# Optimization experiments

Hardware: AMD Instinct MI355X
Metric: run time of the kernel (lower is better)

Reference implementation:

```python
import jax, jax.numpy as jnp
import numpy as np

RES = 7          # pooler_resolution
SR = 2           # sampling_ratio
SCALES = (0.25, 0.125, 0.0625)  # 1/stride for the 3 FPN levels


def _bilinear(feat, ys, xs):
    # feat [C,H,W]; ys, xs [N,S,S] sample coords; returns [C,N,S,S]
    C, H, W = feat.shape
    valid = (ys > -1.0) & (ys < H) & (xs > -1.0) & (xs < W)
    y = jnp.clip(ys, 0.0, H - 1)
    x = jnp.clip(xs, 0.0, W - 1)
    y0 = jnp.floor(y).astype(jnp.int32)
    x0 = jnp.floor(x).astype(jnp.int32)
    y1 = jnp.minimum(y0 + 1, H - 1)
    x1 = jnp.minimum(x0 + 1, W - 1)
    ly = y - y0; lx = x - x0
    hy = 1.0 - ly; hx = 1.0 - lx
    v = (feat[:, y0, x0] * (hy * hx) + feat[:, y0, x1] * (hy * lx)
         + feat[:, y1, x0] * (ly * hx) + feat[:, y1, x1] * (ly * lx))
    return v * valid


def _roi_align(feat, boxes, scale):
    # feat [C,H,W], boxes [N,4] (t,l,b,r) in image coords, aligned=True
    t, l, b, r = (boxes[:, 0], boxes[:, 1], boxes[:, 2], boxes[:, 3])
    sy = t * scale - 0.5
    sx = l * scale - 0.5
    bh = (b - t) * scale / RES
    bw = (r - l) * scale / RES
    S = RES * SR
    g = (jnp.arange(S, dtype=feat.dtype) + 0.5) / SR  # sample offsets in bin units
    ys = sy[:, None] + g[None, :] * bh[:, None]  # [N,S]
    xs = sx[:, None] + g[None, :] * bw[:, None]
    N = boxes.shape[0]
    Y = jnp.broadcast_to(ys[:, :, None], (N, S, S))
    X = jnp.broadcast_to(xs[:, None, :], (N, S, S))
    v = _bilinear(feat, Y, X)                      # [C,N,S,S]
    C = feat.shape[0]
    v = v.reshape(C, N, RES, SR, RES, SR).mean(axis=(3, 5))
    return jnp.transpose(v, (1, 0, 2, 3))          # [N,C,RES,RES]


def _forward(feat0, feat1, feat2, bbox2d, anchor_id,
             fc1_w, fc1_b, bn1_g, bn1_b, fc2_w, fc2_b, bn2_g, bn2_b,
             cate_w, cate_b, bbox3d_w, bbox3d_b, yawc_w, yawc_b,
             yawr_w, yawr_b, hgt_w, hgt_b):
    # yxhw -> tlbr (mu.convert_box_format_yxhw_to_tlbr)
    cy, cx, h, w = (bbox2d[..., 0], bbox2d[..., 1], bbox2d[..., 2], bbox2d[..., 3])
    tlbr = jnp.stack([cy - h / 2, cx - w / 2, cy + h / 2, cx + w / 2], axis=-1)
    level = anchor_id // 3  # [B,N] per-box FPN level (anchor_id // 3 == i routing)
    feats = [feat0, feat1, feat2]
    B, N = level.shape
    C = feat0.shape[1]
    pooled = jnp.zeros((B, N, C, RES, RES), dtype=feat0.dtype)
    for i in range(3):
        al = jax.vmap(lambda fm, bx, s=SCALES[i]: _roi_align(fm, bx, s))(feats[i], tlbr)
        pooled = jnp.where((level == i)[:, :, None, None, None], al, pooled)
    x = pooled.reshape(B * N, -1)  # [B*N, C*RES*RES]
    eps = 1e-5
    for Wt, bb, g2, b2 in ((fc1_w, fc1_b, bn1_g, bn1_b), (fc2_w, fc2_b, bn2_g, bn2_b)):
        x = x @ Wt + bb
        mu = x.mean(0)
        var = x.var(0)
        x = jax.nn.relu((x - mu) / jnp.sqrt(var + eps) * g2 + b2)
    cate = x @ cate_w + cate_b
    bbox3d = x @ bbox3d_w + bbox3d_b
    yawc = x @ yawc_w + yawc_b
    yawr = x @ yawr_w + yawr_b
    hgt = x @ hgt_w + hgt_b
    out = jnp.concatenate([cate, bbox3d, yawc, yawr, hgt], axis=-1)  # [B*N, 100]
    return out.reshape(B, N, -1)


def setup_inputs() -> dict:
    key = jax.random.key(0)
    ks = jax.random.split(key, 24)
    B, N, C = 4, 512, 256
    FC = 1024
    IMG = 512.0
    NUM_CLASSES, BOX_DIM, BINS = 3, 6, 12
    feat0 = jax.random.normal(ks[0], (B, C, 128, 128), jnp.float32)
    feat1 = jax.random.normal(ks[1], (B, C, 64, 64), jnp.float32)
    feat2 = jax.random.normal(ks[2], (B, C, 32, 32), jnp.float32)
    cy = jax.random.uniform(ks[3], (B, N)) * IMG
    cx = jax.random.uniform(ks[4], (B, N)) * IMG
    h = 16.0 + jax.random.uniform(ks[5], (B, N)) * 240.0
    w = 16.0 + jax.random.uniform(ks[6], (B, N)) * 240.0
    bbox2d = jnp.stack([cy, cx, h, w], axis=-1)
    anchor_id = jax.random.randint(ks[7], (B, N), 0, 9, dtype=jnp.int32)
    in_dim = C * RES * RES  # 12544
    fc1_w = jax.random.normal(ks[8], (in_dim, FC), jnp.float32) / np.sqrt(in_dim)
    fc1_b = jnp.zeros((FC,), jnp.float32)
    bn1_g = jnp.ones((FC,), jnp.float32)
    bn1_b = jnp.zeros((FC,), jnp.float32)
    fc2_w = jax.random.normal(ks[9], (FC, FC), jnp.float32) / np.sqrt(FC)
    fc2_b = jnp.zeros((FC,), jnp.float32)
    bn2_g = jnp.ones((FC,), jnp.float32)
    bn2_b = jnp.zeros((FC,), jnp.float32)
    cate_w = jax.random.normal(ks[10], (FC, NUM_CLASSES + 1), jnp.float32) * 0.01
    cate_b = jnp.zeros((NUM_CLASSES + 1,), jnp.float32)
    bbox3d_w = jax.random.normal(ks[11], (FC, NUM_CLASSES * BOX_DIM), jnp.float32) * 0.001
    bbox3d_b = jnp.zeros((NUM_CLASSES * BOX_DIM,), jnp.float32)
    yawc_w = jax.random.normal(ks[12], (FC, NUM_CLASSES * BINS), jnp.float32) * 0.001
    yawc_b = jnp.zeros((NUM_CLASSES * BINS,), jnp.float32)
    yawr_w = jax.random.normal(ks[13], (FC, NUM_CLASSES * BINS), jnp.float32) * 0.001
    yawr_b = jnp.zeros((NUM_CLASSES * BINS,), jnp.float32)
    hgt_w = jax.random.normal(ks[14], (FC, NUM_CLASSES * 2), jnp.float32) * 0.001
    hgt_b = jnp.zeros((NUM_CLASSES * 2,), jnp.float32)
    return {
        'feat0': feat0, 'feat1': feat1, 'feat2': feat2,
        'bbox2d': bbox2d, 'anchor_id': anchor_id,
        'fc1_w': fc1_w, 'fc1_b': fc1_b, 'bn1_g': bn1_g, 'bn1_b': bn1_b,
        'fc2_w': fc2_w, 'fc2_b': fc2_b, 'bn2_g': bn2_g, 'bn2_b': bn2_b,
        'cate_w': cate_w, 'cate_b': cate_b, 'bbox3d_w': bbox3d_w, 'bbox3d_b': bbox3d_b,
        'yawc_w': yawc_w, 'yawc_b': yawc_b, 'yawr_w': yawr_w, 'yawr_b': yawr_b,
        'hgt_w': hgt_w, 'hgt_b': hgt_b,
    }


def reference(feat0, feat1, feat2, bbox2d, anchor_id,
              fc1_w, fc1_b, bn1_g, bn1_b, fc2_w, fc2_b, bn2_g, bn2_b,
              cate_w, cate_b, bbox3d_w, bbox3d_b, yawc_w, yawc_b,
              yawr_w, yawr_b, hgt_w, hgt_b):
    return _forward(feat0, feat1, feat2, bbox2d, anchor_id,
                    fc1_w, fc1_b, bn1_g, bn1_b, fc2_w, fc2_b, bn2_g, bn2_b,
                    cate_w, cate_b, bbox3d_w, bbox3d_b, yawc_w, yawc_b,
                    yawr_w, yawr_b, hgt_w, hgt_b)
```

## Files before the change

kernel.cpp:

```cpp
#include <hip/hip_runtime.h>
#include <hip/hip_bf16.h>

typedef unsigned short u16;
typedef unsigned int u32;
typedef __bf16 bf16x8 __attribute__((ext_vector_type(8)));
typedef float f32x4 __attribute__((ext_vector_type(4)));

#define RESOLUTION 7
#define SR 2
#define SS 14
#define NSAMP 196

static __device__ __forceinline__ u16 f2bf(float f) {
    __hip_bfloat16 t = __float2bfloat16(f);
    return *reinterpret_cast<u16*>(&t);
}
static __device__ __forceinline__ float bf2f(u16 h) {
    return __uint_as_float(((u32)h) << 16);
}

static __device__ __forceinline__ void load_lds16(const u16* g, u16* l) {
    __builtin_amdgcn_global_load_lds(
        (const __attribute__((address_space(1))) unsigned int*)g,
        (__attribute__((address_space(3))) unsigned int*)l, 16, 0, 0);
}

__global__ __launch_bounds__(256) void transpose_feat3_kernel(
    const float* __restrict__ f0, const float* __restrict__ f1,
    const float* __restrict__ f2, u16* __restrict__ tf0,
    u16* __restrict__ tf1, u16* __restrict__ tf2) {
    int b = blockIdx.y;
    int bx = blockIdx.x;
    const float* in;
    u16* out;
    int HW, hw0;
    if (bx < 256)      { in = f0; out = tf0; HW = 16384; hw0 = bx * 64; }
    else if (bx < 320) { in = f1; out = tf1; HW = 4096;  hw0 = (bx - 256) * 64; }
    else               { in = f2; out = tf2; HW = 1024;  hw0 = (bx - 320) * 64; }

    __shared__ u16 tile[256][65];
    int hw4 = (threadIdx.x & 15) * 4;
    int cs = threadIdx.x >> 4;
    for (int cc = 0; cc < 256; cc += 16) {
        int c = cc + cs;
        float4 v = *(const float4*)&in[((size_t)(b * 256 + c)) * HW + hw0 + hw4];
        tile[c][hw4 + 0] = f2bf(v.x);
        tile[c][hw4 + 1] = f2bf(v.y);
        tile[c][hw4 + 2] = f2bf(v.z);
        tile[c][hw4 + 3] = f2bf(v.w);
    }
    __syncthreads();

    int ro = threadIdx.x >> 5;
    int co = (threadIdx.x & 31) * 8;
    for (int i = 0; i < 64; i += 8) {
        int hw = i + ro;
        union { uint4 v; u16 h[8]; } o;
        #pragma unroll
        for (int j = 0; j < 8; ++j) o.h[j] = tile[co + j][hw];
        *(uint4*)&out[((size_t)b * HW + hw0 + hw) * 256 + co] = o.v;
    }
}

__global__ __launch_bounds__(256) void transpose_w_kernel(
    const float* __restrict__ in, u16* __restrict__ out, int K, int perm) {
    int kp0 = blockIdx.x * 64, n0 = blockIdx.y * 64;
    __shared__ u16 tile[64][65];

    int nn4 = (threadIdx.x & 15) * 4;
    int ks = threadIdx.x >> 4;
    for (int i = 0; i < 64; i += 16) {
        int kp = kp0 + ks + i;
        int k = perm ? ((kp & 255) * 49 + (kp >> 8)) : kp;
        float4 v = *(const float4*)&in[(size_t)k * 1024 + n0 + nn4];
        tile[ks + i][nn4 + 0] = f2bf(v.x);
        tile[ks + i][nn4 + 1] = f2bf(v.y);
        tile[ks + i][nn4 + 2] = f2bf(v.z);
        tile[ks + i][nn4 + 3] = f2bf(v.w);
    }
    __syncthreads();

    int nw = threadIdx.x >> 3, ko = (threadIdx.x & 7) * 8;
    for (int i = 0; i < 2; ++i) {
        int n = nw + i * 32;
        union { uint4 v; u16 h[8]; } o;
        #pragma unroll
        for (int j = 0; j < 8; ++j) o.h[j] = tile[ko + j][n];
        *(uint4*)&out[(size_t)(n0 + n) * K + kp0 + ko] = o.v;
    }
}

__global__ void head_concat_kernel(
    const float* __restrict__ cate_w, const float* __restrict__ bbox3d_w,
    const float* __restrict__ yawc_w, const float* __restrict__ yawr_w,
    const float* __restrict__ hgt_w,
    const float* __restrict__ cate_b, const float* __restrict__ bbox3d_b,
    const float* __restrict__ yawc_b, const float* __restrict__ yawr_b,
    const float* __restrict__ hgt_b,
    u16* __restrict__ whT, float* __restrict__ bh) {
    int idx = blockIdx.x * blockDim.x + threadIdx.x;
    if (idx < 128 * 1024) {
        int n = idx >> 10, k = idx & 1023;
        float v = 0.f;
        if (n < 4)        v = cate_w[k * 4 + n];
        else if (n < 22)  v = bbox3d_w[k * 18 + (n - 4)];
        else if (n < 58)  v = yawc_w[k * 36 + (n - 22)];
        else if (n < 94)  v = yawr_w[k * 36 + (n - 58)];
        else if (n < 100) v = hgt_w[k * 6 + (n - 94)];
        whT[idx] = f2bf(v);
    }
    if (idx < 100) {
        int c = idx;
        float v;
        if (c < 4)        v = cate_b[c];
        else if (c < 22)  v = bbox3d_b[c - 4];
        else if (c < 58)  v = yawc_b[c - 22];
        else if (c < 94)  v = yawr_b[c - 58];
        else              v = hgt_b[c - 94];
        bh[c] = v;
    }
}

__global__ __launch_bounds__(512) void roi_align_v3_kernel(
    const u16* __restrict__ tf0, const u16* __restrict__ tf1,
    const u16* __restrict__ tf2, const float* __restrict__ bbox2d,
    const int* __restrict__ anchor_id, u16* __restrict__ xb) {
    int bn = blockIdx.x;
    int b = bn >> 9;
    int tid = threadIdx.x;

    __shared__ int s_o00[NSAMP], s_o01[NSAMP], s_o10[NSAMP], s_o11[NSAMP];
    __shared__ float s_w00[NSAMP], s_w01[NSAMP], s_w10[NSAMP], s_w11[NSAMP];

    float cy = bbox2d[bn * 4 + 0], cx = bbox2d[bn * 4 + 1];
    float hh = bbox2d[bn * 4 + 2], ww = bbox2d[bn * 4 + 3];
    int lvl = anchor_id[bn] / 3;
    float scale = (lvl == 0) ? 0.25f : ((lvl == 1) ? 0.125f : 0.0625f);
    int H = (lvl == 0) ? 128 : ((lvl == 1) ? 64 : 32);
    int W = H;

    float t = cy - hh * 0.5f, l = cx - ww * 0.5f;
    float btm = cy + hh * 0.5f, r = cx + ww * 0.5f;
    float sy = t * scale - 0.5f, sx = l * scale - 0.5f;
    float bh = (btm - t) * scale * (1.0f / RESOLUTION);
    float bw = (r - l) * scale * (1.0f / RESOLUTION);

    if (tid < NSAMP) {
        int i = tid / SS, j = tid % SS;
        float gi = (i + 0.5f) * (1.0f / SR);
        float gj = (j + 0.5f) * (1.0f / SR);
        float y = sy + gi * bh, x = sx + gj * bw;
        float valid = (y > -1.0f && y < (float)H && x > -1.0f && x < (float)W)
                          ? 0.25f : 0.0f;
        y = fminf(fmaxf(y, 0.0f), (float)(H - 1));
        x = fminf(fmaxf(x, 0.0f), (float)(W - 1));
        int y0 = (int)floorf(y), x0 = (int)floorf(x);
        int y1 = min(y0 + 1, H - 1), x1 = min(x0 + 1, W - 1);
        float ly = y - (float)y0, lx = x - (float)x0;
        float hy = 1.f - ly, hx = 1.f - lx;
        s_o00[tid] = (y0 * W + x0) * 256;
        s_o01[tid] = (y0 * W + x1) * 256;
        s_o10[tid] = (y1 * W + x0) * 256;
        s_o11[tid] = (y1 * W + x1) * 256;
        s_w00[tid] = hy * hx * valid;
        s_w01[tid] = hy * lx * valid;
        s_w10[tid] = ly * hx * valid;
        s_w11[tid] = ly * lx * valid;
    }
    __syncthreads();

    const u16* fb = (lvl == 0) ? (tf0 + (size_t)b * 16384 * 256)
                  : (lvl == 1) ? (tf1 + (size_t)b * 4096 * 256)
                               : (tf2 + (size_t)b * 1024 * 256);
    int g = tid >> 5;
    int c0 = (tid & 31) * 8;
    u16* xr = xb + (size_t)bn * 12544;

    #pragma unroll
    for (int ii = 0; ii < 4; ++ii) {
        int bin = g + ii * 16;
        if (bin < 49) {
            int ph = bin / 7, pw = bin % 7;
            float a[8] = {0.f, 0.f, 0.f, 0.f, 0.f, 0.f, 0.f, 0.f};
            #pragma unroll
            for (int dy = 0; dy < SR; ++dy) {
                #pragma unroll
                for (int dx = 0; dx < SR; ++dx) {
                    int si = (ph * SR + dy) * SS + (pw * SR + dx);
                    int o00 = s_o00[si], o01 = s_o01[si];
                    int o10 = s_o10[si], o11 = s_o11[si];
                    float w00 = s_w00[si], w01 = s_w01[si];
                    float w10 = s_w10[si], w11 = s_w11[si];
                    union { uint4 v; u16 h[8]; } u0, u1, u2, u3;
                    u0.v = *(const uint4*)(fb + o00 + c0);
                    u1.v = *(const uint4*)(fb + o01 + c0);
                    u2.v = *(const uint4*)(fb + o10 + c0);
                    u3.v = *(const uint4*)(fb + o11 + c0);
                    #pragma unroll
                    for (int j = 0; j < 8; ++j) {
                        a[j] = fmaf(bf2f(u0.h[j]), w00, a[j]);
                        a[j] = fmaf(bf2f(u1.h[j]), w01, a[j]);
                        a[j] = fmaf(bf2f(u2.h[j]), w10, a[j]);
                        a[j] = fmaf(bf2f(u3.h[j]), w11, a[j]);
                    }
                }
            }
            union { uint4 v; u16 h[8]; } o;
            #pragma unroll
            for (int j = 0; j < 8; ++j) o.h[j] = f2bf(a[j]);
            *(uint4*)&xr[bin * 256 + c0] = o.v;
        }
    }
}

__global__ void bias_out_init_kernel(float* __restrict__ out,
                                     const float* __restrict__ bh, int total) {
    int idx = blockIdx.x * blockDim.x + threadIdx.x;
    if (idx >= total) return;
    int m = idx / 100, n = idx - m * 100;
    out[idx] = bh[n];
}

__global__ __launch_bounds__(256) void gemm_splitk_kernel(
    const u16* __restrict__ A, const u16* __restrict__ BT,
    float* __restrict__ Y, int ldY, int nmax, int K, int KC) {
    __shared__ u16 la[2][128 * 32];
    __shared__ u16 lb[2][128 * 32];
    int m0 = blockIdx.x * 128;
    int n0 = blockIdx.y * 128;
    int kbeg = blockIdx.z * KC;
    int tid = threadIdx.x;
    int w = tid >> 6, lane = tid & 63;
    int wm = (w >> 1) * 64, wn = (w & 1) * 64;

    int idx1 = tid + 256;
    const u16* gA0 = A + (size_t)(m0 + (tid >> 2)) * K + (tid & 3) * 8 + kbeg;
    const u16* gA1 = A + (size_t)(m0 + (idx1 >> 2)) * K + (idx1 & 3) * 8 + kbeg;
    const u16* gB0 = BT + (size_t)(n0 + (tid >> 2)) * K + (tid & 3) * 8 + kbeg;
    const u16* gB1 = BT + (size_t)(n0 + (idx1 >> 2)) * K + (idx1 & 3) * 8 + kbeg;
    u16* lA0a = la[0] + w * 512;
    u16* lA1a = la[0] + 2048 + w * 512;
    u16* lB0a = lb[0] + w * 512;
    u16* lB1a = lb[0] + 2048 + w * 512;
    u16* lA0b = la[1] + w * 512;
    u16* lA1b = la[1] + 2048 + w * 512;
    u16* lB0b = lb[1] + w * 512;
    u16* lB1b = lb[1] + 2048 + w * 512;

    f32x4 acc[4][4] = {};
    int row16 = lane & 15, q8 = (lane >> 4) * 8;

    for (int k0 = 0; k0 < KC; k0 += 64) {
        load_lds16(gA0 + k0, lA0a);
        load_lds16(gA1 + k0, lA1a);
        load_lds16(gB0 + k0, lB0a);
        load_lds16(gB1 + k0, lB1a);
        load_lds16(gA0 + k0 + 32, lA0b);
        load_lds16(gA1 + k0 + 32, lA1b);
        load_lds16(gB0 + k0 + 32, lB0b);
        load_lds16(gB1 + k0 + 32, lB1b);
        __syncthreads();

        #pragma unroll
        for (int h = 0; h < 2; ++h) {
            bf16x8 af[4], bf[4];
            #pragma unroll
            for (int tm = 0; tm < 4; ++tm)
                af[tm] = *(const bf16x8*)&la[h][(wm + tm * 16 + row16) * 32 + q8];
            #pragma unroll
            for (int tn = 0; tn < 4; ++tn)
                bf[tn] = *(const bf16x8*)&lb[h][(wn + tn * 16 + row16) * 32 + q8];
            #pragma unroll
            for (int tm = 0; tm < 4; ++tm)
                #pragma unroll
                for (int tn = 0; tn < 4; ++tn)
                    acc[tm][tn] = __builtin_amdgcn_mfma_f32_16x16x32_bf16(
                        af[tm], bf[tn], acc[tm][tn], 0, 0, 0);
        }
        __syncthreads();
    }

    int col = lane & 15, qr = lane >> 4;
    #pragma unroll
    for (int tm = 0; tm < 4; ++tm) {
        #pragma unroll
        for (int tn = 0; tn < 4; ++tn) {
            int nn = n0 + wn + tn * 16 + col;
            if (nn < nmax) {
                #pragma unroll
                for (int rg = 0; rg < 4; ++rg) {
                    int mm = m0 + wm + tm * 16 + qr * 4 + rg;
                    unsafeAtomicAdd(&Y[(size_t)mm * ldY + nn], acc[tm][tn][rg]);
                }
            }
        }
    }
}

__global__ __launch_bounds__(256) void bn_stats_part_kernel(
    const float* __restrict__ y, float* __restrict__ part, int N) {
    int c4 = blockIdx.x * 256 + (threadIdx.x & 63) * 4;
    int rg = threadIdx.x >> 6;
    int r0 = blockIdx.y * 32;
    float4 s = make_float4(0.f, 0.f, 0.f, 0.f);
    float4 q = make_float4(0.f, 0.f, 0.f, 0.f);
    for (int i = 0; i < 8; ++i) {
        int r = r0 + rg + i * 4;
        float4 v = *(const float4*)&y[(size_t)r * N + c4];
        s.x += v.x; s.y += v.y; s.z += v.z; s.w += v.w;
        q.x += v.x * v.x; q.y += v.y * v.y; q.z += v.z * v.z; q.w += v.w * v.w;
    }
    __shared__ float4 ls[4][64], lq[4][64];
    ls[rg][threadIdx.x & 63] = s;
    lq[rg][threadIdx.x & 63] = q;
    __syncthreads();
    if (rg == 0) {
        int cx = threadIdx.x & 63;
        #pragma unroll
        for (int g = 1; g < 4; ++g) {
            float4 a = ls[g][cx], b = lq[g][cx];
            s.x += a.x; s.y += a.y; s.z += a.z; s.w += a.w;
            q.x += b.x; q.y += b.y; q.z += b.z; q.w += b.w;
        }
        float* po = part + (size_t)blockIdx.y * 2048;
        *(float4*)&po[c4] = s;
        *(float4*)&po[1024 + c4] = q;
    }
}

__global__ __launch_bounds__(256) void bn_stats_final_kernel(
    const float* __restrict__ part, float* __restrict__ stats, int M, int nchunk) {
    int col = blockIdx.x * 256 + threadIdx.x;
    float s = 0.f, q = 0.f;
    for (int ch = 0; ch < nchunk; ++ch) {
        s += part[(size_t)ch * 2048 + col];
        q += part[(size_t)ch * 2048 + 1024 + col];
    }
    float mean = s / (float)M;
    float var = q / (float)M - mean * mean;
    stats[col] = mean;
    stats[1024 + col] = rsqrtf(var + 1e-5f);
}

__global__ void bn_apply_kernel(float* __restrict__ y,
                                const float* __restrict__ stats,
                                const float* __restrict__ g,
                                const float* __restrict__ b,
                                u16* __restrict__ xo, int total4, int zero_y) {
    int idx = blockIdx.x * blockDim.x + threadIdx.x;
    if (idx >= total4) return;
    int e0 = idx * 4;
    int col = e0 & 1023;
    float4 v = *(const float4*)&y[e0];
    float4 mu = *(const float4*)&stats[col];
    float4 rs = *(const float4*)&stats[1024 + col];
    float4 gg = *(const float4*)&g[col];
    float4 bb = *(const float4*)&b[col];
    ushort4 o;
    o.x = f2bf(fmaxf((v.x - mu.x) * rs.x * gg.x + bb.x, 0.f));
    o.y = f2bf(fmaxf((v.y - mu.y) * rs.y * gg.y + bb.y, 0.f));
    o.z = f2bf(fmaxf((v.z - mu.z) * rs.z * gg.z + bb.z, 0.f));
    o.w = f2bf(fmaxf((v.w - mu.w) * rs.w * gg.w + bb.w, 0.f));
    *(ushort4*)&xo[e0] = o;
    if (zero_y)
        *(float4*)&y[e0] = make_float4(0.f, 0.f, 0.f, 0.f);
}

extern "C" void kernel_launch(void* const* d_in, const int* in_sizes, int n_in,
                              void* d_out, int out_size, void* d_ws, size_t ws_size,
                              hipStream_t stream) {
    const float* feat0   = (const float*)d_in[0];
    const float* feat1   = (const float*)d_in[1];
    const float* feat2   = (const float*)d_in[2];
    const float* bbox2d  = (const float*)d_in[3];
    const int*   anchor  = (const int*)d_in[4];
    const float* fc1_w   = (const float*)d_in[5];
    const float* bn1_g   = (const float*)d_in[7];
    const float* bn1_b   = (const float*)d_in[8];
    const float* fc2_w   = (const float*)d_in[9];
    const float* bn2_g   = (const float*)d_in[11];
    const float* bn2_b   = (const float*)d_in[12];
    const float* cate_w  = (const float*)d_in[13];
    const float* cate_b  = (const float*)d_in[14];
    const float* bbox3d_w= (const float*)d_in[15];
    const float* bbox3d_b= (const float*)d_in[16];
    const float* yawc_w  = (const float*)d_in[17];
    const float* yawc_b  = (const float*)d_in[18];
    const float* yawr_w  = (const float*)d_in[19];
    const float* yawr_b  = (const float*)d_in[20];
    const float* hgt_w   = (const float*)d_in[21];
    const float* hgt_b   = (const float*)d_in[22];

    const int B = 4, N = 512, FC = 1024;
    const int M = B * N;
    const int K1 = 12544;

    char* base = (char*)d_ws;
    u16* xb = (u16*)base;
    char* ub = base + 51380224;
    u16* tf0 = (u16*)ub;
    u16* tf1 = (u16*)(ub + 33554432);
    u16* tf2 = (u16*)(ub + 41943040);
    u16* w1t = (u16*)ub;
    u16* w2t = (u16*)(ub + 25690112);
    float* y   = (float*)(ub + 27787264);
    u16* x1b = (u16*)(ub + 36175872);
    float* part = (float*)(ub + 40370176);
    char* tail = ub + 44040192;
    float* stats = (float*)tail;
    u16*   whT   = (u16*)(tail + 8192);
    float* bhd   = (float*)(tail + 8192 + 262144);
    float* outp  = (float*)d_out;

    head_concat_kernel<<<(128 * 1024 + 255) / 256, 256, 0, stream>>>(
        cate_w, bbox3d_w, yawc_w, yawr_w, hgt_w,
        cate_b, bbox3d_b, yawc_b, yawr_b, hgt_b, whT, bhd);

    transpose_feat3_kernel<<<dim3(336, B), 256, 0, stream>>>(
        feat0, feat1, feat2, tf0, tf1, tf2);

    roi_align_v3_kernel<<<M, 512, 0, stream>>>(tf0, tf1, tf2, bbox2d, anchor, xb);

    transpose_w_kernel<<<dim3(K1 / 64, FC / 64), 256, 0, stream>>>(fc1_w, w1t, K1, 1);
    transpose_w_kernel<<<dim3(FC / 64, FC / 64), 256, 0, stream>>>(fc2_w, w2t, FC, 0);

    hipMemsetAsync(y, 0, (size_t)M * FC * 4, stream);
    gemm_splitk_kernel<<<dim3(M / 128, FC / 128, 7), 256, 0, stream>>>(
        xb, w1t, y, FC, FC, K1, K1 / 7);
    bn_stats_part_kernel<<<dim3(FC / 256, M / 32), 256, 0, stream>>>(y, part, FC);
    bn_stats_final_kernel<<<FC / 256, 256, 0, stream>>>(part, stats, M, M / 32);
    bn_apply_kernel<<<(M * FC / 4 + 255) / 256, 256, 0, stream>>>(
        y, stats, bn1_g, bn1_b, x1b, M * FC / 4, 1);

    gemm_splitk_kernel<<<dim3(M / 128, FC / 128, 4), 256, 0, stream>>>(
        x1b, w2t, y, FC, FC, FC, FC / 4);
    bn_stats_part_kernel<<<dim3(FC / 256, M / 32), 256, 0, stream>>>(y, part, FC);
    bn_stats_final_kernel<<<FC / 256, 256, 0, stream>>>(part, stats, M, M / 32);
    bn_apply_kernel<<<(M * FC / 4 + 255) / 256, 256, 0, stream>>>(
        y, stats, bn2_g, bn2_b, x1b, M * FC / 4, 0);

    bias_out_init_kernel<<<(M * 100 + 255) / 256, 256, 0, stream>>>(outp, bhd, M * 100);
    gemm_splitk_kernel<<<dim3(M / 128, 1, 16), 256, 0, stream>>>(
        x1b, whT, outp, 100, 100, FC, FC / 16);
}
```

Measured before the change: 474.1 us.

## Add 256x256 split-K MFMA GEMM with swizzled LDS for fc1

Adds a new 512-thread GEMM kernel that computes a 256x256 output tile per block with a K step of 64, XOR-swizzled LDS layout and double buffering through direct global-to-LDS loads, then uses it for the large fc1 GEMM. Each tile gains operand reuse and issues fewer global loads per FLOP than the 128x128 kernel, and setprio is used around the MFMA bursts. In exchange it uses 128 KB of LDS and many accumulator registers, so only one block fits per CU. It also launches fewer blocks, which risks underfilling the GPU for this M.

```diff
diff --git a/kernel.cpp b/kernel.cpp
--- a/kernel.cpp
+++ b/kernel.cpp
@@ -219,6 +219,99 @@
     if (idx >= total) return;
     int m = idx / 100, n = idx - m * 100;
     out[idx] = bh[n];
+}
+
+__global__ __launch_bounds__(512) void gemm_256_splitk_kernel(
+    const u16* __restrict__ A, const u16* __restrict__ BT,
+    float* __restrict__ Y, int ldY, int K, int KC) {
+    __shared__ __align__(16) u16 lsA[2][256 * 64];
+    __shared__ __align__(16) u16 lsB[2][256 * 64];
+    int m0 = blockIdx.x * 256, n0 = blockIdx.y * 256;
+    int kbeg = blockIdx.z * KC;
+    int tid = threadIdx.x;
+    int wv = tid >> 6, lane = tid & 63;
+    int wm = wv >> 2, wn = wv & 3;
+
+    int sr = tid >> 3, sp = tid & 7;
+    int scol = (sp ^ (sr & 7)) * 8;
+    const u16* gA = A + (size_t)(m0 + sr) * K + kbeg + scol;
+    const u16* gB = BT + (size_t)(n0 + sr) * K + kbeg + scol;
+    int ldst = wv * 8 * 64;
+
+    int aRow = wm * 128 + (lane & 15);
+    int bRow = wn * 64 + (lane & 15);
+    int ps0 = (((lane >> 4)) ^ (lane & 7)) * 8;
+    int ps1 = (((lane >> 4) | 4) ^ (lane & 7)) * 8;
+
+    f32x4 acc[8][4] = {};
+    int NT = KC >> 6;
+
+    #pragma unroll
+    for (int c = 0; c < 4; ++c) {
+        load_lds16(gA + (size_t)(c * 64) * K, &lsA[0][c * 4096 + ldst]);
+        load_lds16(gB + (size_t)(c * 64) * K, &lsB[0][c * 4096 + ldst]);
+    }
+    __syncthreads();
+
+    for (int kt = 0; kt < NT; ++kt) {
+        int b = kt & 1;
+        if (kt + 1 < NT) {
+            int ko = (kt + 1) << 6;
+            #pragma unroll
+            for (int c = 0; c < 4; ++c) {
+                load_lds16(gA + (size_t)(c * 64) * K + ko, &lsA[b ^ 1][c * 4096 + ldst]);
+                load_lds16(gB + (size_t)(c * 64) * K + ko, &lsB[b ^ 1][c * 4096 + ldst]);
+            }
+        }
+        bf16x8 bfr[4][2];
+        #pragma unroll
+        for (int ni = 0; ni < 4; ++ni) {
+            bfr[ni][0] = *(const bf16x8*)&lsB[b][(bRow + ni * 16) * 64 + ps0];
+            bfr[ni][1] = *(const bf16x8*)&lsB[b][(bRow + ni * 16) * 64 + ps1];
+        }
+        #pragma unroll
+        for (int q = 0; q < 4; ++q) {
+            bf16x8 af[2][2];
+            #pragma unroll
+            for (int m2 = 0; m2 < 2; ++m2) {
+                int rr = (aRow + (q * 2 + m2) * 16) * 64;
+                af[m2][0] = *(const bf16x8*)&lsA[b][rr + ps0];
+                af[m2][1] = *(const bf16x8*)&lsA[b][rr + ps1];
+            }
+            __builtin_amdgcn_s_setprio(1);
+            #pragma unroll
+            for (int m2 = 0; m2 < 2; ++m2) {
+                #pragma unroll
+                for (int ni = 0; ni < 4; ++ni) {
+                    acc[q * 2 + m2][ni] = __builtin_amdgcn_mfma_f32_16x16x32_bf16(
+                        af[m2][0], bfr[ni][0], acc[q * 2 + m2][ni], 0, 0, 0);
+                    acc[q * 2 + m2][ni] = __builtin_amdgcn_mfma_f32_16x16x32_bf16(
+                        af[m2][1], bfr[ni][1], acc[q * 2 + m2][ni], 0, 0, 0);
+                }
+            }
+            __builtin_amdgcn_s_setprio(0);
+            if (q < 3) {
+                asm volatile("" ::: "memory");
+                __builtin_amdgcn_s_barrier();
+                asm volatile("" ::: "memory");
+            }
+        }
+        __syncthreads();
+    }
+
+    int col = lane & 15, qr = lane >> 4;
+    #pragma unroll
+    for (int mi = 0; mi < 8; ++mi) {
+        #pragma unroll
+        for (int ni = 0; ni < 4; ++ni) {
+            int nn = n0 + wn * 64 + ni * 16 + col;
+            #pragma unroll
+            for (int rg = 0; rg < 4; ++rg) {
+                int mm = m0 + wm * 128 + mi * 16 + qr * 4 + rg;
+                unsafeAtomicAdd(&Y[(size_t)mm * ldY + nn], acc[mi][ni][rg]);
+            }
+        }
+    }
 }
 
 __global__ __launch_bounds__(256) void gemm_splitk_kernel(
@@ -425,8 +518,8 @@
     transpose_w_kernel<<<dim3(FC / 64, FC / 64), 256, 0, stream>>>(fc2_w, w2t, FC, 0);
 
     hipMemsetAsync(y, 0, (size_t)M * FC * 4, stream);
-    gemm_splitk_kernel<<<dim3(M / 128, FC / 128, 7), 256, 0, stream>>>(
-        xb, w1t, y, FC, FC, K1, K1 / 7);
+    gemm_256_splitk_kernel<<<dim3(M / 256, FC / 256, 7), 512, 0, stream>>>(
+        xb, w1t, y, FC, K1, K1 / 7);
     bn_stats_part_kernel<<<dim3(FC / 256, M / 32), 256, 0, stream>>>(y, part, FC);
     bn_stats_final_kernel<<<FC / 256, 256, 0, stream>>>(part, stats, M, M / 32);
     bn_apply_kernel<<<(M * FC / 4 + 255) / 256, 256, 0, stream>>>(
```

Result: faster. 462.4 us (-2.5%).
